# Optimization experiments

Hardware: AMD Instinct MI355X
Metric: run time of the kernel (lower is better)

The kernel has to match this reference:

```python
import jax, jax.numpy as jnp
import numpy as np

BN_EPS = 1e-5


def setup_inputs() -> dict:
    key = jax.random.key(0)
    ks = jax.random.split(key, 11)
    C, P = 256, 128  # inplanes, planes = inplanes // 2
    B, H, W = 4, 64, 64
    s = 0.01  # conv weight init std in the original module
    return {
        "x": jax.random.normal(ks[0], (B, C, H, W), jnp.float32),
        "Wt": jax.random.normal(ks[1], (P, C), jnp.float32) * s,
        "bt": jnp.zeros((P,), jnp.float32),
        "Wp": jax.random.normal(ks[2], (P, C), jnp.float32) * s,
        "bp": jnp.zeros((P,), jnp.float32),
        "Wg": jax.random.normal(ks[3], (P, C), jnp.float32) * s,
        "bg": jnp.zeros((P,), jnp.float32),
        "Wz": jax.random.normal(ks[4], (C, P), jnp.float32) * s,
        "bz": jnp.zeros((C,), jnp.float32),
        "gamma": jax.random.uniform(ks[5], (C,), jnp.float32),
        "beta": jax.random.normal(ks[6], (C,), jnp.float32) * 0.01,
    }


def reference(x, Wt, bt, Wp, bp, Wg, bg, Wz, bz, gamma, beta):
    b, c, h, w = x.shape
    n = h * w
    xf = x.reshape(b, c, n)  # (b, c, n)
    # 1x1 conv projections == per-pixel matmuls
    t = jnp.einsum("pc,bcn->bnp", Wt, xf) + bt            # (b, n, p) queries
    p = jnp.einsum("pc,bcn->bpn", Wp, xf) + bp[:, None]   # (b, p, n) keys
    g = jnp.einsum("pc,bcn->bnp", Wg, xf) + bg            # (b, n, p) values
    planes = Wt.shape[0]
    scale = jnp.asarray(planes, x.dtype) ** 0.5
    att = jnp.einsum("bnp,bpm->bnm", t, p) / scale        # (b, n, n)
    att = jax.nn.softmax(att, axis=-1)                    # softmax over dim 2
    y = jnp.einsum("bnm,bmp->bnp", att, g)                # (b, n, p)
    z = jnp.einsum("cp,bnp->bcn", Wz, y) + bz[:, None]    # (b, c, n)
    z = z.reshape(b, c, h, w)
    # BatchNorm2d, training-mode batch statistics over (B, H, W)
    mean = z.mean(axis=(0, 2, 3))
    var = z.var(axis=(0, 2, 3))
    zn = (z - mean[:, None, None]) * jax.lax.rsqrt(var + BN_EPS)[:, None, None]
    out = zn * gamma[:, None, None] + beta[:, None, None] + x
    return out
```

## Files before the change

### kernel.cpp

```cpp
#include <hip/hip_runtime.h>


#define SCALE_ 0.08838834764831845f
#define QSCALE_ 2.0404384761599213f

typedef __bf16 bf16x8 __attribute__((ext_vector_type(8)));
typedef float f32x4 __attribute__((ext_vector_type(4)));
typedef unsigned short ushort8v __attribute__((ext_vector_type(8)));
typedef long long llx2 __attribute__((ext_vector_type(2)));

__device__ inline unsigned short f2bf(float f) {
  unsigned int u = __float_as_uint(f);
  u += 0x7fffu + ((u >> 16) & 1u);
  return (unsigned short)(u >> 16);
}
__device__ inline float bflo(unsigned int u) { return __uint_as_float(u << 16); }
__device__ inline float bfhi(unsigned int u) { return __uint_as_float(u & 0xffff0000u); }

__device__ inline unsigned char f2fp8(float f) {
  unsigned u = __float_as_uint(f);
  unsigned sign = (u >> 24) & 0x80u;
  unsigned a = u & 0x7fffffffu;
  if (a >= 0x43E00000u) return (unsigned char)(sign | 0x7Eu);
  if (a >= 0x3C800000u) {
    unsigned r = a + 0x0007FFFFu + ((a >> 20) & 1u);
    r &= 0xFFF00000u;
    int e8 = (int)((r >> 23) & 0xFFu) - 120;
    unsigned m3 = (r >> 20) & 7u;
    return (unsigned char)(sign | ((unsigned)e8 << 3) | m3);
  }
  float q = __uint_as_float(a) * 512.0f;
  int d = (int)rintf(q);
  if (d >= 8) return (unsigned char)(sign | 0x08u);
  return (unsigned char)(sign | (unsigned)d);
}

__device__ inline void gl16(const void* g, void* l) {
  __builtin_amdgcn_global_load_lds(
      (const __attribute__((address_space(1))) unsigned int*)(g),
      (__attribute__((address_space(3))) unsigned int*)(l), 16, 0, 0);
}

__global__ __launch_bounds__(256) void prep_kernel(
    const float* __restrict__ x,
    const float* __restrict__ Wt, const float* __restrict__ Wp, const float* __restrict__ Wg,
    unsigned short* __restrict__ xT, unsigned short* __restrict__ Wb) {
  const int tid = threadIdx.x;
  const int bx = blockIdx.x, b = blockIdx.y;
  if (bx >= 64) {
    if (b != 0) return;
#pragma unroll
    for (int it = 0; it < 3; ++it) {
      int k = (bx - 64) * 256 + tid + it * 4096;
      const float* src = (k < 4096 ? Wt : (k < 8192 ? Wp : Wg)) + (size_t)(k & 4095) * 8;
      float4 a = *(const float4*)src, c = *(const float4*)(src + 4);
      ushort8v us;
      us[0] = f2bf(a.x); us[1] = f2bf(a.y); us[2] = f2bf(a.z); us[3] = f2bf(a.w);
      us[4] = f2bf(c.x); us[5] = f2bf(c.y); us[6] = f2bf(c.z); us[7] = f2bf(c.w);
      *(ushort8v*)(Wb + (size_t)k * 8) = us;
    }
    return;
  }
  __shared__ float sT[128 * 68];
  const int w = tid >> 6, l = tid & 63;
  const int n0 = bx * 64;
  for (int half = 0; half < 2; ++half) {
    if (half) __syncthreads();
#pragma unroll
    for (int it = 0; it < 8; ++it) {
      int e = it * 256 + tid;
      int c = e >> 4, n4 = e & 15;
      float4 v = *(const float4*)(x + (size_t)(b * 256 + half * 128 + c) * 4096 + n0 + n4 * 4);
      *(float4*)(sT + c * 68 + n4 * 4) = v;
    }
    __syncthreads();
#pragma unroll
    for (int it = 0; it < 4; ++it) {
      int c8 = it * 4 + w;
      int n = l;
      ushort8v us;
#pragma unroll
      for (int j = 0; j < 8; ++j) us[j] = f2bf(sT[(c8 * 8 + j) * 68 + n]);
      *(ushort8v*)(xT + (size_t)b * 1048576 + (size_t)(n0 + n) * 256 + half * 128 + c8 * 8) = us;
    }
  }
}

__global__ __launch_bounds__(256, 3) void proj_kernel(
    const unsigned short* __restrict__ xT, const unsigned short* __restrict__ Wb,
    const float* __restrict__ bt, const float* __restrict__ bp, const float* __restrict__ bg,
    unsigned char* __restrict__ Qb8, unsigned char* __restrict__ Kb8,
    unsigned char* __restrict__ Vtb8) {
  __shared__ unsigned short sX[64 * 256];
  __shared__ unsigned short sW[128 * 64];
  const int tid = threadIdx.x;
  const int w = tid >> 6, l = tid & 63;
  const int l15 = l & 15, lh = l >> 4;
  const int n0 = blockIdx.x * 64;
  const int b = blockIdx.y;
  const int sel = blockIdx.z;
  const unsigned short* xTb = xT + (size_t)b * 1048576;
  const unsigned short* Ws = Wb + (size_t)sel * 32768;
#pragma unroll
  for (int it = 0; it < 8; ++it) {
    int row = w * 16 + it * 2 + (l >> 5);
    int s = l & 31;
    int src = (s & 24) | ((s & 7) ^ (row & 7));
    gl16(xTb + (size_t)(n0 + row) * 256 + src * 8, sX + (w * 16 + it * 2) * 256);
  }
  f32x4 acc[2][4];
#pragma unroll
  for (int mt = 0; mt < 2; ++mt)
#pragma unroll
    for (int nt = 0; nt < 4; ++nt) acc[mt][nt] = (f32x4){0.f, 0.f, 0.f, 0.f};

  for (int ko4 = 0; ko4 < 4; ++ko4) {
    __syncthreads();
#pragma unroll
    for (int it = 0; it < 4; ++it) {
      int p = w * 32 + it * 8 + (l >> 3);
      int s = l & 7;
      gl16(Ws + (size_t)p * 256 + ko4 * 64 + ((s ^ (p & 7)) * 8),
           sW + (w * 32 + it * 8) * 64);
    }
    __syncthreads();
#pragma unroll
    for (int ko2 = 0; ko2 < 2; ++ko2) {
      bf16x8 af[2];
#pragma unroll
      for (int mt = 0; mt < 2; ++mt) {
        int p = w * 32 + mt * 16 + l15;
        af[mt] = *(const bf16x8*)(sW + p * 64 + (((ko2 * 4 + lh) ^ (p & 7)) << 3));
      }
#pragma unroll
      for (int nt = 0; nt < 4; ++nt) {
        int n = nt * 16 + l15;
        int ci = ko4 * 8 + ko2 * 4 + lh;
        int slot = (ci & 24) | ((ci & 7) ^ (n & 7));
        bf16x8 bfv = *(const bf16x8*)(sX + n * 256 + (slot << 3));
#pragma unroll
        for (int mt = 0; mt < 2; ++mt)
          acc[mt][nt] = __builtin_amdgcn_mfma_f32_16x16x32_bf16(af[mt], bfv, acc[mt][nt], 0, 0, 0);
      }
    }
  }
  const float* bias = sel == 0 ? bt : (sel == 1 ? bp : bg);
  const float scl = sel == 0 ? QSCALE_ : 1.0f;
#pragma unroll
  for (int mt = 0; mt < 2; ++mt) {
    int pb = w * 32 + mt * 16 + lh * 4;
    float4 bv = *(const float4*)(bias + pb);
    const float* bvf = (const float*)&bv;
    if (sel < 2) {
      unsigned char* dst = (sel == 0 ? Qb8 : Kb8) + (size_t)b * 524288;
#pragma unroll
      for (int nt = 0; nt < 4; ++nt) {
        uchar4 us;
        us.x = f2fp8((acc[mt][nt][0] + bv.x) * scl);
        us.y = f2fp8((acc[mt][nt][1] + bv.y) * scl);
        us.z = f2fp8((acc[mt][nt][2] + bv.z) * scl);
        us.w = f2fp8((acc[mt][nt][3] + bv.w) * scl);
        *(uchar4*)(dst + (size_t)(n0 + nt * 16 + l15) * 128 + pb) = us;
      }
    } else {
      unsigned char* dst = Vtb8 + (size_t)b * 524288;
#pragma unroll
      for (int nt = 0; nt < 4; ++nt)
#pragma unroll
        for (int r = 0; r < 4; ++r)
          dst[(size_t)(pb + r) * 4096 + n0 + nt * 16 + l15] = f2fp8(acc[mt][nt][r] + bvf[r]);
    }
  }
}

__global__ __launch_bounds__(256, 3) void attn_kernel(
    const unsigned char* __restrict__ Qb8, const unsigned char* __restrict__ Kb8,
    const unsigned char* __restrict__ Vtb8, unsigned short* __restrict__ Ytp,
    float* __restrict__ denp) {
  __shared__ f32x4 smq[2560];
  unsigned char* sm = (unsigned char*)smq;
  const int tid = threadIdx.x;
  const int w = tid >> 6, l = tid & 63;
  const int l15 = l & 15, lh = l >> 4;
  const int b = blockIdx.y, sp = blockIdx.z;
  const int n0 = blockIdx.x * 128;
  const int kvbase = sp * 1024;

  long long qf0[4], qf1[4];
  {
    const unsigned char* q0 = Qb8 + (size_t)(b * 4096 + n0 + w * 32 + l15) * 128 + lh * 32;
    const unsigned char* q1 = q0 + 16 * 128;
#pragma unroll
    for (int ko = 0; ko < 4; ++ko) {
      qf0[ko] = *(const long long*)(q0 + ko * 8);
      qf1[ko] = *(const long long*)(q1 + ko * 8);
    }
  }
  unsigned char* sPw = sm + 32768 + w * 2048;

  f32x4 yacc0[8], yacc1[8];
#pragma unroll
  for (int i = 0; i < 8; ++i) {
    yacc0[i] = (f32x4){0.f, 0.f, 0.f, 0.f};
    yacc1[i] = (f32x4){0.f, 0.f, 0.f, 0.f};
  }
  float den0 = 0.f, den1 = 0.f;

  const unsigned char* Kbase = Kb8 + (size_t)(b * 4096 + kvbase) * 128;
  const unsigned char* Vbase = Vtb8 + (size_t)(b * 128) * 4096 + kvbase;

#define STAGE(T, BUFO)                                                               \
  {                                                                                  \
    const int koff_ = (T) * 64;                                                      \
    _Pragma("unroll")                                                                \
    for (int it = 0; it < 2; ++it) {                                                 \
      int krow = w * 16 + it * 8 + (l >> 3);                                         \
      gl16(Kbase + (size_t)(koff_ + krow) * 128 + (((l & 7) ^ (krow & 7)) << 4),     \
           sm + (BUFO) + (w * 16 + it * 8) * 128);                                   \
      int vrow = w * 32 + it * 16 + (l >> 2);                                        \
      gl16(Vbase + (size_t)vrow * 4096 + koff_ + (((l & 3) ^ (vrow & 3)) << 4),      \
           sm + 16384 + (BUFO) + (w * 32 + it * 16) * 64);                           \
    }                                                                                \
  }

  STAGE(0, 0)
  for (int t = 0; t < 16; ++t) {
    const int co = (t & 1) * 8192;
    unsigned char* kb = sm + co;
    unsigned char* vb = sm + 16384 + co;
    __syncthreads();
    if (t + 1 < 16) {
      STAGE(t + 1, co ^ 8192)
    }
    f32x4 sacc0[4], sacc1[4];
#pragma unroll
    for (int mt = 0; mt < 4; ++mt) {
      sacc0[mt] = (f32x4){0.f, 0.f, 0.f, 0.f};
      sacc1[mt] = (f32x4){0.f, 0.f, 0.f, 0.f};
    }
    __builtin_amdgcn_s_setprio(1);
#pragma unroll
    for (int mt = 0; mt < 4; ++mt) {
      int m = mt * 16 + l15;
      llx2 k01 = *(const llx2*)(kb + m * 128 + (((lh * 2 + 0) ^ (m & 7)) << 4));
      llx2 k23 = *(const llx2*)(kb + m * 128 + (((lh * 2 + 1) ^ (m & 7)) << 4));
      sacc0[mt] = __builtin_amdgcn_mfma_f32_16x16x32_fp8_fp8(k01[0], qf0[0], sacc0[mt], 0, 0, 0);
      sacc1[mt] = __builtin_amdgcn_mfma_f32_16x16x32_fp8_fp8(k01[0], qf1[0], sacc1[mt], 0, 0, 0);
      sacc0[mt] = __builtin_amdgcn_mfma_f32_16x16x32_fp8_fp8(k01[1], qf0[1], sacc0[mt], 0, 0, 0);
      sacc1[mt] = __builtin_amdgcn_mfma_f32_16x16x32_fp8_fp8(k01[1], qf1[1], sacc1[mt], 0, 0, 0);
      sacc0[mt] = __builtin_amdgcn_mfma_f32_16x16x32_fp8_fp8(k23[0], qf0[2], sacc0[mt], 0, 0, 0);
      sacc1[mt] = __builtin_amdgcn_mfma_f32_16x16x32_fp8_fp8(k23[0], qf1[2], sacc1[mt], 0, 0, 0);
      sacc0[mt] = __builtin_amdgcn_mfma_f32_16x16x32_fp8_fp8(k23[1], qf0[3], sacc0[mt], 0, 0, 0);
      sacc1[mt] = __builtin_amdgcn_mfma_f32_16x16x32_fp8_fp8(k23[1], qf1[3], sacc1[mt], 0, 0, 0);
    }
    __builtin_amdgcn_s_setprio(0);
#define SOFTMAX_SET(SACC, ROWB, DEN)                                                 \
    {                                                                                \
      float rs = 0.f;                                                                \
      _Pragma("unroll")                                                              \
      for (int mt = 0; mt < 4; ++mt) {                                               \
        float e0 = __builtin_amdgcn_exp2f(SACC[mt][0] * 0.0625f);                    \
        float e1 = __builtin_amdgcn_exp2f(SACC[mt][1] * 0.0625f);                    \
        float e2 = __builtin_amdgcn_exp2f(SACC[mt][2] * 0.0625f);                    \
        float e3 = __builtin_amdgcn_exp2f(SACC[mt][3] * 0.0625f);                    \
        rs += (e0 + e1) + (e2 + e3);                                                 \
        int pk = __builtin_amdgcn_cvt_pk_fp8_f32(e0, e1, 0, false);                  \
        pk = __builtin_amdgcn_cvt_pk_fp8_f32(e2, e3, pk, true);                      \
        *(int*)(sPw + ((ROWB) + l15) * 64 + ((mt ^ (l15 & 3)) << 4) + lh * 4) = pk;  \
      }                                                                              \
      rs += __shfl_xor(rs, 16);                                                      \
      rs += __shfl_xor(rs, 32);                                                      \
      DEN += rs;                                                                     \
    }
    SOFTMAX_SET(sacc0, 0, den0)
    SOFTMAX_SET(sacc1, 16, den1)
    __builtin_amdgcn_s_setprio(1);
    {
      llx2 bp0 = *(const llx2*)(sPw + l15 * 64 + ((lh ^ (l15 & 3)) << 4));
      llx2 bp1 = *(const llx2*)(sPw + (16 + l15) * 64 + ((lh ^ (l15 & 3)) << 4));
#pragma unroll
      for (int dt = 0; dt < 8; ++dt) {
        int d = dt * 16 + l15;
        llx2 av = *(const llx2*)(vb + d * 64 + ((lh ^ (d & 3)) << 4));
        yacc0[dt] = __builtin_amdgcn_mfma_f32_16x16x32_fp8_fp8(av[0], bp0[0], yacc0[dt], 0, 0, 0);
        yacc1[dt] = __builtin_amdgcn_mfma_f32_16x16x32_fp8_fp8(av[0], bp1[0], yacc1[dt], 0, 0, 0);
        yacc0[dt] = __builtin_amdgcn_mfma_f32_16x16x32_fp8_fp8(av[1], bp0[1], yacc0[dt], 0, 0, 0);
        yacc1[dt] = __builtin_amdgcn_mfma_f32_16x16x32_fp8_fp8(av[1], bp1[1], yacc1[dt], 0, 0, 0);
      }
    }
    __builtin_amdgcn_s_setprio(0);
  }
  {
    unsigned short* Yt = Ytp + (size_t)(sp * 4 + b) * 524288 +
                         (size_t)(n0 + w * 32 + l15) * 128;
#pragma unroll
    for (int dt = 0; dt < 8; ++dt) {
      ushort4 us;
      us.x = f2bf(yacc0[dt][0]); us.y = f2bf(yacc0[dt][1]);
      us.z = f2bf(yacc0[dt][2]); us.w = f2bf(yacc0[dt][3]);
      *(ushort4*)(Yt + dt * 16 + lh * 4) = us;
    }
    unsigned short* Yt1 = Yt + 16 * 128;
#pragma unroll
    for (int dt = 0; dt < 8; ++dt) {
      ushort4 us;
      us.x = f2bf(yacc1[dt][0]); us.y = f2bf(yacc1[dt][1]);
      us.z = f2bf(yacc1[dt][2]); us.w = f2bf(yacc1[dt][3]);
      *(ushort4*)(Yt1 + dt * 16 + lh * 4) = us;
    }
    if (lh == 0) {
      denp[(size_t)(sp * 4 + b) * 4096 + n0 + w * 32 + l15] = den0;
      denp[(size_t)(sp * 4 + b) * 4096 + n0 + w * 32 + 16 + l15] = den1;
    }
  }
}

__global__ __launch_bounds__(256, 4) void zbn_kernel(
    const unsigned short* __restrict__ Ytp, const float* __restrict__ denp,
    const float* __restrict__ Wz, const float* __restrict__ bz,
    unsigned short* __restrict__ Zb, float* __restrict__ S1p, float* __restrict__ S2p) {
  __shared__ unsigned short sY[64 * 128];
  __shared__ unsigned short sW[64 * 128];
  __shared__ float sDen[64];
  const int tid = threadIdx.x;
  const int w = tid >> 6, l = tid & 63;
  const int l15 = l & 15, lh = l >> 4;
  const int bx = blockIdx.x;
  const int b = blockIdx.y;
  const int n0 = bx * 64;
  const int c0 = blockIdx.z * 64;
  if (tid < 64) {
    float s = 0.f;
#pragma unroll
    for (int sp = 0; sp < 4; ++sp) s += denp[sp * 16384 + b * 4096 + n0 + tid];
    sDen[tid] = 1.0f / s;
  }
  __syncthreads();
#pragma unroll
  for (int it = 0; it < 4; ++it) {
    int e = it * 256 + tid;
    int n = e >> 4, pc = e & 15;
    size_t o = (size_t)b * 524288 + (size_t)(n0 + n) * 128 + pc * 8;
    float a0 = 0, a1 = 0, a2 = 0, a3 = 0, a4 = 0, a5 = 0, a6 = 0, a7 = 0;
#pragma unroll
    for (int sp = 0; sp < 4; ++sp) {
      uint4 v = *(const uint4*)(Ytp + (size_t)sp * 2097152 + o);
      a0 += bflo(v.x); a1 += bfhi(v.x);
      a2 += bflo(v.y); a3 += bfhi(v.y);
      a4 += bflo(v.z); a5 += bfhi(v.z);
      a6 += bflo(v.w); a7 += bfhi(v.w);
    }
    float idn = sDen[n];
    ushort8v us;
    us[0] = f2bf(a0 * idn); us[1] = f2bf(a1 * idn);
    us[2] = f2bf(a2 * idn); us[3] = f2bf(a3 * idn);
    us[4] = f2bf(a4 * idn); us[5] = f2bf(a5 * idn);
    us[6] = f2bf(a6 * idn); us[7] = f2bf(a7 * idn);
    *(ushort8v*)(sY + n * 128 + ((pc ^ (n & 7)) << 3)) = us;
  }
#pragma unroll
  for (int it = 0; it < 4; ++it) {
    int e = it * 256 + tid;
    int c = e >> 4, pc = e & 15;
    const float* wsrc = Wz + (size_t)(c0 + c) * 128 + pc * 8;
    float4 wa = *(const float4*)(wsrc);
    float4 wb = *(const float4*)(wsrc + 4);
    ushort8v us;
    us[0] = f2bf(wa.x); us[1] = f2bf(wa.y); us[2] = f2bf(wa.z); us[3] = f2bf(wa.w);
    us[4] = f2bf(wb.x); us[5] = f2bf(wb.y); us[6] = f2bf(wb.z); us[7] = f2bf(wb.w);
    *(ushort8v*)(sW + c * 128 + ((pc ^ (c & 7)) << 3)) = us;
  }
  __syncthreads();
  f32x4 acc[4];
#pragma unroll
  for (int nt = 0; nt < 4; ++nt) acc[nt] = (f32x4){0.f, 0.f, 0.f, 0.f};
  const int crow = w * 16 + l15;
#pragma unroll
  for (int ko = 0; ko < 4; ++ko) {
    bf16x8 aw = *(const bf16x8*)(sW + crow * 128 + (((lh + 4 * ko) ^ (crow & 7)) << 3));
#pragma unroll
    for (int nt = 0; nt < 4; ++nt) {
      int nrow = nt * 16 + l15;
      bf16x8 by = *(const bf16x8*)(sY + nrow * 128 + (((lh + 4 * ko) ^ (nrow & 7)) << 3));
      acc[nt] = __builtin_amdgcn_mfma_f32_16x16x32_bf16(aw, by, acc[nt], 0, 0, 0);
    }
  }
  const int cb = c0 + w * 16 + lh * 4;
  float4 bzv = *(const float4*)(bz + cb);
  const float* bzf = (const float*)&bzv;
#pragma unroll
  for (int r = 0; r < 4; ++r) {
    float s1 = 0.f, s2 = 0.f;
#pragma unroll
    for (int nt = 0; nt < 4; ++nt) {
      float z = acc[nt][r] + bzf[r];
      Zb[(size_t)(b * 256 + cb + r) * 4096 + n0 + nt * 16 + l15] = f2bf(z);
      s1 += z;
      s2 += z * z;
    }
#pragma unroll
    for (int m = 1; m < 16; m <<= 1) {
      s1 += __shfl_xor(s1, m);
      s2 += __shfl_xor(s2, m);
    }
    if (l15 == 0) {
      S1p[(size_t)(cb + r) * 256 + b * 64 + bx] = s1;
      S2p[(size_t)(cb + r) * 256 + b * 64 + bx] = s2;
    }
  }
}

__global__ __launch_bounds__(256) void bnfin_kernel(
    const float* __restrict__ S1p, const float* __restrict__ S2p,
    const float* __restrict__ gamma, const float* __restrict__ beta,
    float* __restrict__ Scale, float* __restrict__ Shift) {
  __shared__ float r1[4], r2[4];
  const int c = blockIdx.x, tid = threadIdx.x;
  float s1 = S1p[(size_t)c * 256 + tid];
  float s2 = S2p[(size_t)c * 256 + tid];
#pragma unroll
  for (int m = 1; m < 64; m <<= 1) {
    s1 += __shfl_xor(s1, m);
    s2 += __shfl_xor(s2, m);
  }
  if ((tid & 63) == 0) { r1[tid >> 6] = s1; r2[tid >> 6] = s2; }
  __syncthreads();
  if (tid == 0) {
    float S1t = (r1[0] + r1[1]) + (r1[2] + r1[3]);
    float S2t = (r2[0] + r2[1]) + (r2[2] + r2[3]);
    const float inv_cnt = 1.0f / 16384.0f;
    float mean = S1t * inv_cnt;
    float var = fmaxf(S2t * inv_cnt - mean * mean, 0.0f);
    float inv = rsqrtf(var + 1e-5f);
    float sc = gamma[c] * inv;
    Scale[c] = sc;
    Shift[c] = beta[c] - mean * sc;
  }
}

__global__ __launch_bounds__(256) void out_kernel(
    const unsigned short* __restrict__ Zb, const float* __restrict__ x,
    const float* __restrict__ Scale, const float* __restrict__ Shift,
    float* __restrict__ out) {
  int i8 = blockIdx.x * 256 + threadIdx.x;
  size_t flat = (size_t)i8 * 8;
  int c = ((int)(flat >> 12)) & 255;
  uint4 zv = *(const uint4*)(Zb + flat);
  float4 xa = *(const float4*)(x + flat);
  float4 xb = *(const float4*)(x + flat + 4);
  float sc = Scale[c], sh = Shift[c];
  float4 oa, ob;
  oa.x = bflo(zv.x) * sc + sh + xa.x;
  oa.y = bfhi(zv.x) * sc + sh + xa.y;
  oa.z = bflo(zv.y) * sc + sh + xa.z;
  oa.w = bfhi(zv.y) * sc + sh + xa.w;
  ob.x = bflo(zv.z) * sc + sh + xb.x;
  ob.y = bfhi(zv.z) * sc + sh + xb.y;
  ob.z = bflo(zv.w) * sc + sh + xb.z;
  ob.w = bfhi(zv.w) * sc + sh + xb.w;
  *(float4*)(out + flat) = oa;
  *(float4*)(out + flat + 4) = ob;
}

extern "C" void kernel_launch(void* const* d_in, const int* in_sizes, int n_in,
                              void* d_out, int out_size, void* d_ws, size_t ws_size,
                              hipStream_t stream) {
  (void)in_sizes; (void)n_in; (void)out_size; (void)ws_size;
  const float* x = (const float*)d_in[0];
  const float* Wt = (const float*)d_in[1];
  const float* bt = (const float*)d_in[2];
  const float* Wp = (const float*)d_in[3];
  const float* bp = (const float*)d_in[4];
  const float* Wg = (const float*)d_in[5];
  const float* bg = (const float*)d_in[6];
  const float* Wz = (const float*)d_in[7];
  const float* bz = (const float*)d_in[8];
  const float* gamma = (const float*)d_in[9];
  const float* beta = (const float*)d_in[10];

  unsigned char* Qb8 = (unsigned char*)d_ws;
  unsigned char* Kb8 = Qb8 + 2097152;
  unsigned char* Vtb8 = Kb8 + 2097152;
  unsigned short* Ytp = (unsigned short*)(Vtb8 + 2097152);
  float* denp = (float*)(Ytp + 8388608);
  float* Zr = denp + 65536;
  float* Scale = Zr + 4194304;
  float* Shift = Scale + 256;

  unsigned short* Zb = (unsigned short*)Zr;
  unsigned short* xT = (unsigned short*)Zr;
  unsigned short* Wb = (unsigned short*)denp;
  float* S1p = (float*)Qb8;
  float* S2p = S1p + 65536;

  prep_kernel<<<dim3(80, 4), 256, 0, stream>>>(x, Wt, Wp, Wg, xT, Wb);
  proj_kernel<<<dim3(64, 4, 3), 256, 0, stream>>>(xT, Wb, bt, bp, bg, Qb8, Kb8, Vtb8);
  attn_kernel<<<dim3(32, 4, 4), 256, 0, stream>>>(Qb8, Kb8, Vtb8, Ytp, denp);
  zbn_kernel<<<dim3(64, 4, 4), 256, 0, stream>>>(Ytp, denp, Wz, bz, Zb, S1p, S2p);
  bnfin_kernel<<<256, 256, 0, stream>>>(S1p, S2p, gamma, beta, Scale, Shift);
  out_kernel<<<2048, 256, 0, stream>>>(Zb, x, Scale, Shift, (float*)d_out);
}
```

Measured before the change: 82.39 us.

## Split attention KV into eight chunks and store partial outputs as fp8

Doubles the split-KV factor from 4 to 8, so the attention grid goes from 512 to 1024 blocks, each doing half as many KV tiles. Partial Y results are now written as fp8 through hardware pack conversions instead of bf16, which keeps partial-output traffic near its old size despite twice as many partials. Occupancy is raised to 4 blocks per SM. The reduction in zbn now sums 8 fp8 partials. This risks accuracy loss from fp8 partial outputs that are not normalised, and adds per-block Q-load and epilogue overhead relative to the work done.

New measurement: 116.4 us. +41.3%, slower.

```diff
diff --git a/kernel.cpp b/kernel.cpp
--- a/kernel.cpp
+++ b/kernel.cpp
@@ -173,9 +173,9 @@
   }
 }
 
-__global__ __launch_bounds__(256, 3) void attn_kernel(
+__global__ __launch_bounds__(256, 4) void attn_kernel(
     const unsigned char* __restrict__ Qb8, const unsigned char* __restrict__ Kb8,
-    const unsigned char* __restrict__ Vtb8, unsigned short* __restrict__ Ytp,
+    const unsigned char* __restrict__ Vtb8, unsigned char* __restrict__ Ytp8,
     float* __restrict__ denp) {
   __shared__ f32x4 smq[2560];
   unsigned char* sm = (unsigned char*)smq;
@@ -184,7 +184,7 @@
   const int l15 = l & 15, lh = l >> 4;
   const int b = blockIdx.y, sp = blockIdx.z;
   const int n0 = blockIdx.x * 128;
-  const int kvbase = sp * 1024;
+  const int kvbase = sp * 512;
 
   long long qf0[4], qf1[4];
   {
@@ -224,12 +224,12 @@
   }
 
   STAGE(0, 0)
-  for (int t = 0; t < 16; ++t) {
+  for (int t = 0; t < 8; ++t) {
     const int co = (t & 1) * 8192;
     unsigned char* kb = sm + co;
     unsigned char* vb = sm + 16384 + co;
     __syncthreads();
-    if (t + 1 < 16) {
+    if (t + 1 < 8) {
       STAGE(t + 1, co ^ 8192)
     }
     f32x4 sacc0[4], sacc1[4];
@@ -291,32 +291,30 @@
     __builtin_amdgcn_s_setprio(0);
   }
   {
-    unsigned short* Yt = Ytp + (size_t)(sp * 4 + b) * 524288 +
-                         (size_t)(n0 + w * 32 + l15) * 128;
+    unsigned char* Yt = Ytp8 + (size_t)sp * 2097152 + (size_t)b * 524288 +
+                        (size_t)(n0 + w * 32 + l15) * 128;
 #pragma unroll
     for (int dt = 0; dt < 8; ++dt) {
-      ushort4 us;
-      us.x = f2bf(yacc0[dt][0]); us.y = f2bf(yacc0[dt][1]);
-      us.z = f2bf(yacc0[dt][2]); us.w = f2bf(yacc0[dt][3]);
-      *(ushort4*)(Yt + dt * 16 + lh * 4) = us;
-    }
-    unsigned short* Yt1 = Yt + 16 * 128;
+      int pk = __builtin_amdgcn_cvt_pk_fp8_f32(yacc0[dt][0], yacc0[dt][1], 0, false);
+      pk = __builtin_amdgcn_cvt_pk_fp8_f32(yacc0[dt][2], yacc0[dt][3], pk, true);
+      *(int*)(Yt + dt * 16 + lh * 4) = pk;
+    }
+    unsigned char* Yt1 = Yt + 16 * 128;
 #pragma unroll
     for (int dt = 0; dt < 8; ++dt) {
-      ushort4 us;
-      us.x = f2bf(yacc1[dt][0]); us.y = f2bf(yacc1[dt][1]);
-      us.z = f2bf(yacc1[dt][2]); us.w = f2bf(yacc1[dt][3]);
-      *(ushort4*)(Yt1 + dt * 16 + lh * 4) = us;
+      int pk = __builtin_amdgcn_cvt_pk_fp8_f32(yacc1[dt][0], yacc1[dt][1], 0, false);
+      pk = __builtin_amdgcn_cvt_pk_fp8_f32(yacc1[dt][2], yacc1[dt][3], pk, true);
+      *(int*)(Yt1 + dt * 16 + lh * 4) = pk;
     }
     if (lh == 0) {
-      denp[(size_t)(sp * 4 + b) * 4096 + n0 + w * 32 + l15] = den0;
-      denp[(size_t)(sp * 4 + b) * 4096 + n0 + w * 32 + 16 + l15] = den1;
+      denp[sp * 16384 + b * 4096 + n0 + w * 32 + l15] = den0;
+      denp[sp * 16384 + b * 4096 + n0 + w * 32 + 16 + l15] = den1;
     }
   }
 }
 
 __global__ __launch_bounds__(256, 4) void zbn_kernel(
-    const unsigned short* __restrict__ Ytp, const float* __restrict__ denp,
+    const unsigned char* __restrict__ Ytp8, const float* __restrict__ denp,
     const float* __restrict__ Wz, const float* __restrict__ bz,
     unsigned short* __restrict__ Zb, float* __restrict__ S1p, float* __restrict__ S2p) {
   __shared__ unsigned short sY[64 * 128];
@@ -332,7 +330,7 @@
   if (tid < 64) {
     float s = 0.f;
 #pragma unroll
-    for (int sp = 0; sp < 4; ++sp) s += denp[sp * 16384 + b * 4096 + n0 + tid];
+    for (int sp = 0; sp < 8; ++sp) s += denp[sp * 16384 + b * 4096 + n0 + tid];
     sDen[tid] = 1.0f / s;
   }
   __syncthreads();
@@ -343,12 +341,16 @@
     size_t o = (size_t)b * 524288 + (size_t)(n0 + n) * 128 + pc * 8;
     float a0 = 0, a1 = 0, a2 = 0, a3 = 0, a4 = 0, a5 = 0, a6 = 0, a7 = 0;
 #pragma unroll
-    for (int sp = 0; sp < 4; ++sp) {
-      uint4 v = *(const uint4*)(Ytp + (size_t)sp * 2097152 + o);
-      a0 += bflo(v.x); a1 += bfhi(v.x);
-      a2 += bflo(v.y); a3 += bfhi(v.y);
-      a4 += bflo(v.z); a5 += bfhi(v.z);
-      a6 += bflo(v.w); a7 += bfhi(v.w);
+    for (int sp = 0; sp < 8; ++sp) {
+      uint2 v = *(const uint2*)(Ytp8 + (size_t)sp * 2097152 + o);
+      a0 += __builtin_amdgcn_cvt_f32_fp8(v.x, 0);
+      a1 += __builtin_amdgcn_cvt_f32_fp8(v.x, 1);
+      a2 += __builtin_amdgcn_cvt_f32_fp8(v.x, 2);
+      a3 += __builtin_amdgcn_cvt_f32_fp8(v.x, 3);
+      a4 += __builtin_amdgcn_cvt_f32_fp8(v.y, 0);
+      a5 += __builtin_amdgcn_cvt_f32_fp8(v.y, 1);
+      a6 += __builtin_amdgcn_cvt_f32_fp8(v.y, 2);
+      a7 += __builtin_amdgcn_cvt_f32_fp8(v.y, 3);
     }
     float idn = sDen[n];
     ushort8v us;
@@ -481,9 +483,9 @@
   unsigned char* Qb8 = (unsigned char*)d_ws;
   unsigned char* Kb8 = Qb8 + 2097152;
   unsigned char* Vtb8 = Kb8 + 2097152;
-  unsigned short* Ytp = (unsigned short*)(Vtb8 + 2097152);
-  float* denp = (float*)(Ytp + 8388608);
-  float* Zr = denp + 65536;
+  unsigned char* Ytp8 = Vtb8 + 2097152;
+  float* denp = (float*)(Ytp8 + 16777216);
+  float* Zr = denp + 131072;
   float* Scale = Zr + 4194304;
   float* Shift = Scale + 256;
 
@@ -495,8 +497,8 @@
 
   prep_kernel<<<dim3(80, 4), 256, 0, stream>>>(x, Wt, Wp, Wg, xT, Wb);
   proj_kernel<<<dim3(64, 4, 3), 256, 0, stream>>>(xT, Wb, bt, bp, bg, Qb8, Kb8, Vtb8);
-  attn_kernel<<<dim3(32, 4, 4), 256, 0, stream>>>(Qb8, Kb8, Vtb8, Ytp, denp);
-  zbn_kernel<<<dim3(64, 4, 4), 256, 0, stream>>>(Ytp, denp, Wz, bz, Zb, S1p, S2p);
+  attn_kernel<<<dim3(32, 4, 8), 256, 0, stream>>>(Qb8, Kb8, Vtb8, Ytp8, denp);
+  zbn_kernel<<<dim3(64, 4, 4), 256, 0, stream>>>(Ytp8, denp, Wz, bz, Zb, S1p, S2p);
   bnfin_kernel<<<256, 256, 0, stream>>>(S1p, S2p, gamma, beta, Scale, Shift);
   out_kernel<<<2048, 256, 0, stream>>>(Zb, x, Scale, Shift, (float*)d_out);
 }
```
